# Performance work log

Hardware: AMD Instinct MI355X
Metric: run time of the kernel (lower is better)

## Reference

```python
import jax, jax.numpy as jnp
import numpy as np
from jax import lax

PS = 8  # patch size

def setup_inputs() -> dict:
    key = jax.random.key(0)
    ks = jax.random.split(key, 7)
    dim = 64
    B, H, W = 4, 256, 256
    x = jax.random.normal(ks[0], (B, dim, H, W), dtype=jnp.float32)
    # to_hidden: Conv2d(dim, 6*dim, k=1)
    w_hidden = jax.random.normal(ks[1], (6 * dim, dim, 1, 1), dtype=jnp.float32) * 0.05
    b_hidden = jax.random.normal(ks[2], (6 * dim,), dtype=jnp.float32) * 0.01
    # to_hidden_dw: depthwise Conv2d(6*dim, 6*dim, k=3, pad=1, groups=6*dim)
    w_dw = jax.random.normal(ks[3], (6 * dim, 1, 3, 3), dtype=jnp.float32) * 0.05
    b_dw = jax.random.normal(ks[4], (6 * dim,), dtype=jnp.float32) * 0.01
    # project_out: Conv2d(2*dim, dim, k=1)
    w_out = jax.random.normal(ks[5], (dim, 2 * dim, 1, 1), dtype=jnp.float32) * 0.05
    b_out = jax.random.normal(ks[6], (dim,), dtype=jnp.float32) * 0.01
    return {"x": x, "w_hidden": w_hidden, "b_hidden": b_hidden,
            "w_dw": w_dw, "b_dw": b_dw, "w_out": w_out, "b_out": b_out}

def _conv(x, w, groups=1, padding='VALID'):
    return lax.conv_general_dilated(
        x, w, window_strides=(1, 1), padding=padding,
        dimension_numbers=('NCHW', 'OIHW', 'NCHW'),
        feature_group_count=groups)

def reference(x, w_hidden, b_hidden, w_dw, b_dw, w_out, b_out):
    # 1x1 expansion to 6*dim channels
    hidden = _conv(x, w_hidden) + b_hidden[None, :, None, None]
    # 3x3 depthwise conv (groups == channels)
    dw = _conv(hidden, w_dw, groups=w_dw.shape[0], padding='SAME') + b_dw[None, :, None, None]
    q, k, v = jnp.split(dw, 3, axis=1)  # each (B, 2*dim, H, W)
    B, C, H, W = q.shape
    # raw reshape into (B,C,H/8,W/8,8,8) exactly as torch .reshape on contiguous NCHW
    q_patch = q.reshape(B, C, H // PS, W // PS, PS, PS)
    k_patch = k.reshape(B, C, H // PS, W // PS, PS, PS)
    q_fft = jnp.fft.rfft2(q_patch)
    k_fft = jnp.fft.rfft2(k_patch)
    out = jnp.fft.irfft2(q_fft * k_fft, s=(PS, PS))  # circular conv of q,k patches
    out = out.reshape(B, C, (H // PS) * PS, (W // PS) * PS)
    output = v * out
    output = _conv(output, w_out) + b_out[None, :, None, None]
    return output
```

## Files before the change

kernel.cpp:

```cpp
#include <hip/hip_runtime.h>

#define HW 65536
#define W_IMG 256
#define H_IMG 256
#define CIN 64
#define CHID 384
#define CQK 128

__global__ __launch_bounds__(256) void k1_expand(
    const float* __restrict__ x_base,
    const float* __restrict__ wh,
    const float* __restrict__ bh,
    float* __restrict__ hidden_base,
    size_t x_bstride, size_t hid_bstride)
{
    __shared__ float xs[32][256];
    const float* x = x_base + blockIdx.z * x_bstride;
    float* hidden  = hidden_base + blockIdx.z * hid_bstride;
    const int pxbase = blockIdx.x * 256;
    const int cobase = blockIdx.y * 64;
    const int tid  = threadIdx.x;
    const int lane = tid & 63;
    const int wq   = __builtin_amdgcn_readfirstlane(tid >> 6);
    const int px0  = lane * 4;
    const int cw   = cobase + wq * 16;

    float acc[16][4];
    #pragma unroll
    for (int i = 0; i < 16; ++i)
        #pragma unroll
        for (int j = 0; j < 4; ++j) acc[i][j] = 0.f;

    #pragma unroll
    for (int half = 0; half < 2; ++half) {
        const int cib = half * 32;
        if (half) __syncthreads();
        #pragma unroll
        for (int it = 0; it < 8; ++it) {
            int f4 = it * 256 + tid;
            int ci = f4 >> 6;
            int p4 = f4 & 63;
            *reinterpret_cast<float4*>(&xs[ci][p4 * 4]) =
                *reinterpret_cast<const float4*>(
                    &x[(size_t)(cib + ci) * HW + pxbase + p4 * 4]);
        }
        __syncthreads();

        for (int ci4 = 0; ci4 < 32; ci4 += 4) {
            float4 xv[4];
            #pragma unroll
            for (int u = 0; u < 4; ++u)
                xv[u] = *reinterpret_cast<const float4*>(&xs[ci4 + u][px0]);
            #pragma unroll
            for (int g = 0; g < 4; ++g) {
                #pragma unroll
                for (int i = 0; i < 4; ++i) {
                    float4 wv = *reinterpret_cast<const float4*>(
                        &wh[(size_t)(cw + g * 4 + i) * CIN + cib + ci4]);
                    float wu[4] = {wv.x, wv.y, wv.z, wv.w};
                    #pragma unroll
                    for (int u = 0; u < 4; ++u) {
                        acc[g * 4 + i][0] += wu[u] * xv[u].x;
                        acc[g * 4 + i][1] += wu[u] * xv[u].y;
                        acc[g * 4 + i][2] += wu[u] * xv[u].z;
                        acc[g * 4 + i][3] += wu[u] * xv[u].w;
                    }
                }
            }
        }
    }

    #pragma unroll
    for (int i = 0; i < 16; ++i) {
        int co = cw + i;
        float b = bh[co];
        float4 o;
        o.x = acc[i][0] + b; o.y = acc[i][1] + b;
        o.z = acc[i][2] + b; o.w = acc[i][3] + b;
        *reinterpret_cast<float4*>(&hidden[(size_t)co * HW + pxbase + px0]) = o;
    }
}

__global__ __launch_bounds__(256) void k2_fused(
    const float* __restrict__ hidden_base,
    const float* __restrict__ wdw,
    const float* __restrict__ bdw,
    float* __restrict__ vout_base,
    size_t hid_bstride, size_t vout_bstride)
{
    __shared__ float stg[2][10][260];
    __shared__ float qk[2][8][4][68];

    const float* hidden = hidden_base + blockIdx.z * hid_bstride;
    float* vout         = vout_base + blockIdx.z * vout_bstride;

    const int c  = blockIdx.y;
    const int r0 = blockIdx.x * 8;
    const int tid = threadIdx.x;

    #pragma unroll
    for (int it = 0; it < 5; ++it) {
        int f4  = it * 256 + tid;
        int ch  = f4 / 640;
        int rem = f4 - ch * 640;
        int lr  = rem >> 6;
        int p4  = rem & 63;
        int gr  = r0 - 1 + lr;
        float4 v = make_float4(0.f, 0.f, 0.f, 0.f);
        if ((unsigned)gr < H_IMG)
            v = *reinterpret_cast<const float4*>(
                &hidden[(size_t)(c + ch * CQK) * HW + (size_t)gr * W_IMG + p4 * 4]);
        *reinterpret_cast<float4*>(&stg[ch][lr][p4 * 4]) = v;
    }
    __syncthreads();

    const int w = tid;
    const int segw = w >> 6;
    const int tw   = w & 63;
    #pragma unroll
    for (int ch = 0; ch < 2; ++ch) {
        const float* wv = wdw + (c + ch * CQK) * 9;
        const float bias = bdw[c + ch * CQK];
        const float w0 = wv[0], w1 = wv[1], w2 = wv[2];
        const float w3 = wv[3], w4 = wv[4], w5 = wv[5];
        const float w6 = wv[6], w7 = wv[7], w8 = wv[8];
        const float* S = &stg[ch][0][0];

        float am, a0, ap, bm, b0, bp;
        a0 = S[w];
        am = (w > 0)   ? S[w - 1] : 0.f;
        ap = (w < 255) ? S[w + 1] : 0.f;
        b0 = S[260 + w];
        bm = (w > 0)   ? S[260 + w - 1] : 0.f;
        bp = (w < 255) ? S[260 + w + 1] : 0.f;

        #pragma unroll
        for (int r = 0; r < 8; ++r) {
            const float* Sr = S + (r + 2) * 260;
            float c0 = Sr[w];
            float cm = (w > 0)   ? Sr[w - 1] : 0.f;
            float cp = (w < 255) ? Sr[w + 1] : 0.f;
            float a = bias + am * w0 + a0 * w1 + ap * w2
                           + bm * w3 + b0 * w4 + bp * w5
                           + cm * w6 + c0 * w7 + cp * w8;
            qk[ch][r][segw][tw] = a;
            am = bm; a0 = b0; ap = bp;
            bm = cm; b0 = c0; bp = cp;
        }
    }
    __syncthreads();

    const int row = tid >> 5;
    const int seg = (tid >> 3) & 3;
    const int i   = tid & 7;
    const int gr  = r0 + row;
    const int wp0 = seg * 64 + i * 8;

    const float* hbv = hidden + (size_t)(c + 2 * CQK) * HW;
    float4 hv[3][2];
    float  hm[3], hp[3];
    #pragma unroll
    for (int ky = 0; ky < 3; ++ky) {
        int grr = gr + ky - 1;
        hv[ky][0] = make_float4(0.f, 0.f, 0.f, 0.f);
        hv[ky][1] = make_float4(0.f, 0.f, 0.f, 0.f);
        hm[ky] = 0.f; hp[ky] = 0.f;
        if ((unsigned)grr < H_IMG) {
            const float* rb = hbv + (size_t)grr * W_IMG;
            hv[ky][0] = *reinterpret_cast<const float4*>(&rb[wp0]);
            hv[ky][1] = *reinterpret_cast<const float4*>(&rb[wp0 + 4]);
            hm[ky] = (wp0 > 0)   ? rb[wp0 - 1] : 0.f;
            hp[ky] = (wp0 < 248) ? rb[wp0 + 8] : 0.f;
        }
    }

    const float* qb = &qk[0][row][seg][0];
    const float* kb = &qk[1][row][seg][0];

    float acc[8];
    #pragma unroll
    for (int j = 0; j < 8; ++j) acc[j] = 0.f;

    #pragma unroll
    for (int s = 0; s < 8; ++s) {
        int qr = (i - s) & 7;
        float4 ka = *reinterpret_cast<const float4*>(&kb[s * 8]);
        float4 kc = *reinterpret_cast<const float4*>(&kb[s * 8 + 4]);
        float4 qa = *reinterpret_cast<const float4*>(&qb[qr * 8]);
        float4 qc = *reinterpret_cast<const float4*>(&qb[qr * 8 + 4]);
        float kr[8] = {ka.x, ka.y, ka.z, ka.w, kc.x, kc.y, kc.z, kc.w};
        float qv[8] = {qa.x, qa.y, qa.z, qa.w, qc.x, qc.y, qc.z, qc.w};
        #pragma unroll
        for (int t = 0; t < 8; ++t)
            #pragma unroll
            for (int j = 0; j < 8; ++j)
                acc[j] += kr[t] * qv[(j - t) & 7];
    }

    const float* wvv = wdw + (c + 2 * CQK) * 9;
    const float vbias = bdw[c + 2 * CQK];
    float vc[8];
    #pragma unroll
    for (int j = 0; j < 8; ++j) vc[j] = vbias;
    #pragma unroll
    for (int ky = 0; ky < 3; ++ky) {
        float kw0 = wvv[ky * 3], kw1 = wvv[ky * 3 + 1], kw2 = wvv[ky * 3 + 2];
        float h[10];
        h[0] = hm[ky];
        h[1] = hv[ky][0].x; h[2] = hv[ky][0].y; h[3] = hv[ky][0].z; h[4] = hv[ky][0].w;
        h[5] = hv[ky][1].x; h[6] = hv[ky][1].y; h[7] = hv[ky][1].z; h[8] = hv[ky][1].w;
        h[9] = hp[ky];
        #pragma unroll
        for (int j = 0; j < 8; ++j)
            vc[j] += h[j] * kw0 + h[j + 1] * kw1 + h[j + 2] * kw2;
    }

    float* dst = &vout[(size_t)c * HW + (size_t)gr * W_IMG + wp0];
    float4 o0, o1;
    o0.x = acc[0] * vc[0]; o0.y = acc[1] * vc[1];
    o0.z = acc[2] * vc[2]; o0.w = acc[3] * vc[3];
    o1.x = acc[4] * vc[4]; o1.y = acc[5] * vc[5];
    o1.z = acc[6] * vc[6]; o1.w = acc[7] * vc[7];
    *reinterpret_cast<float4*>(dst)     = o0;
    *reinterpret_cast<float4*>(dst + 4) = o1;
}

__global__ __launch_bounds__(256) void k3_project(
    const float* __restrict__ vout_base,
    const float* __restrict__ wo,
    const float* __restrict__ bo,
    float* __restrict__ out_base,
    size_t vout_bstride, size_t out_bstride)
{
    __shared__ float vsh[CQK][64];
    const float* vout = vout_base + blockIdx.z * vout_bstride;
    float* out        = out_base + blockIdx.z * out_bstride;
    const int pxbase = blockIdx.x * 64;
    const int tid  = threadIdx.x;
    const int lane = tid & 63;
    const int wq   = __builtin_amdgcn_readfirstlane(tid >> 6);
    const int cw   = wq * 16;

    #pragma unroll
    for (int it = 0; it < 8; ++it) {
        int f4 = it * 256 + tid;
        int cc = f4 >> 4;
        int p4 = f4 & 15;
        *reinterpret_cast<float4*>(&vsh[cc][p4 * 4]) =
            *reinterpret_cast<const float4*>(&vout[(size_t)cc * HW + pxbase + p4 * 4]);
    }
    __syncthreads();

    float acc[16];
    #pragma unroll
    for (int i = 0; i < 16; ++i) acc[i] = 0.f;

    for (int cc4 = 0; cc4 < CQK; cc4 += 4) {
        float xv[4];
        #pragma unroll
        for (int u = 0; u < 4; ++u)
            xv[u] = vsh[cc4 + u][lane];
        #pragma unroll
        for (int g = 0; g < 4; ++g) {
            #pragma unroll
            for (int i = 0; i < 4; ++i) {
                float4 wv = *reinterpret_cast<const float4*>(
                    &wo[(size_t)(cw + g * 4 + i) * CQK + cc4]);
                acc[g * 4 + i] += wv.x * xv[0] + wv.y * xv[1]
                                + wv.z * xv[2] + wv.w * xv[3];
            }
        }
    }

    #pragma unroll
    for (int i = 0; i < 16; ++i) {
        int co = cw + i;
        out[(size_t)co * HW + pxbase + lane] = acc[i] + bo[co];
    }
}

extern "C" void kernel_launch(void* const* d_in, const int* in_sizes, int n_in,
                              void* d_out, int out_size, void* d_ws, size_t ws_size,
                              hipStream_t stream) {
    const float* x   = (const float*)d_in[0];
    const float* wh  = (const float*)d_in[1];
    const float* bh  = (const float*)d_in[2];
    const float* wdw = (const float*)d_in[3];
    const float* bdw = (const float*)d_in[4];
    const float* wo  = (const float*)d_in[5];
    const float* bo  = (const float*)d_in[6];
    float* out = (float*)d_out;

    const size_t n_hid  = (size_t)CHID * HW;
    const size_t n_vout = (size_t)CQK * HW;
    const size_t n_x    = (size_t)CIN * HW;

    if (ws_size >= 4 * (n_hid + n_vout) * sizeof(float)) {
        float* hidden = (float*)d_ws;
        float* vout   = hidden + 4 * n_hid;
        k1_expand <<<dim3(HW / 256, CHID / 64, 4), 256, 0, stream>>>(
            x, wh, bh, hidden, n_x, n_hid);
        k2_fused  <<<dim3(H_IMG / 8, CQK, 4),      256, 0, stream>>>(
            hidden, wdw, bdw, vout, n_hid, n_vout);
        k3_project<<<dim3(HW / 64, 1, 4),          256, 0, stream>>>(
            vout, wo, bo, out, n_vout, n_x);
    } else {
        float* hidden = (float*)d_ws;
        float* vout   = hidden + n_hid;
        for (int b = 0; b < 4; ++b) {
            const float* xb = x + (size_t)b * n_x;
            float* ob       = out + (size_t)b * n_x;
            k1_expand <<<dim3(HW / 256, CHID / 64, 1), 256, 0, stream>>>(
                xb, wh, bh, hidden, 0, 0);
            k2_fused  <<<dim3(H_IMG / 8, CQK, 1),      256, 0, stream>>>(
                hidden, wdw, bdw, vout, 0, 0);
            k3_project<<<dim3(HW / 64, 1, 1),          256, 0, stream>>>(
                vout, wo, bo, ob, 0, 0);
        }
    }
}
```

Measured before the change: 464.2 us.

## Drop LDS staging in 1x1 convs and read inputs directly from global

Both pointwise conv kernels (expand and project) stop staging input tiles in shared memory with barriers. Each thread now loads its float4 pixel columns straight from global memory inside the channel loop. The project kernel is also reworked so each thread computes 4 pixels × 16 output channels, with 256 pixels per block and a quarter as many blocks, plus float4 stores. This removes LDS traffic and synchronization, relying on L1/L2 caching for the reuse across the four waves that share pixels. The trade-off is more global load instructions and higher register pressure.

```diff
diff --git a/kernel.cpp b/kernel.cpp
--- a/kernel.cpp
+++ b/kernel.cpp
@@ -14,7 +14,6 @@
     float* __restrict__ hidden_base,
     size_t x_bstride, size_t hid_bstride)
 {
-    __shared__ float xs[32][256];
     const float* x = x_base + blockIdx.z * x_bstride;
     float* hidden  = hidden_base + blockIdx.z * hid_bstride;
     const int pxbase = blockIdx.x * 256;
@@ -22,7 +21,7 @@
     const int tid  = threadIdx.x;
     const int lane = tid & 63;
     const int wq   = __builtin_amdgcn_readfirstlane(tid >> 6);
-    const int px0  = lane * 4;
+    const int px   = pxbase + lane * 4;
     const int cw   = cobase + wq * 16;
 
     float acc[16][4];
@@ -31,41 +30,23 @@
         #pragma unroll
         for (int j = 0; j < 4; ++j) acc[i][j] = 0.f;
 
-    #pragma unroll
-    for (int half = 0; half < 2; ++half) {
-        const int cib = half * 32;
-        if (half) __syncthreads();
-        #pragma unroll
-        for (int it = 0; it < 8; ++it) {
-            int f4 = it * 256 + tid;
-            int ci = f4 >> 6;
-            int p4 = f4 & 63;
-            *reinterpret_cast<float4*>(&xs[ci][p4 * 4]) =
-                *reinterpret_cast<const float4*>(
-                    &x[(size_t)(cib + ci) * HW + pxbase + p4 * 4]);
-        }
-        __syncthreads();
-
-        for (int ci4 = 0; ci4 < 32; ci4 += 4) {
-            float4 xv[4];
+    #pragma unroll 2
+    for (int ci4 = 0; ci4 < CIN; ci4 += 4) {
+        float4 xv[4];
+        #pragma unroll
+        for (int u = 0; u < 4; ++u)
+            xv[u] = *reinterpret_cast<const float4*>(&x[(size_t)(ci4 + u) * HW + px]);
+        #pragma unroll
+        for (int i = 0; i < 16; ++i) {
+            float4 wv = *reinterpret_cast<const float4*>(
+                &wh[(size_t)(cw + i) * CIN + ci4]);
+            float wu[4] = {wv.x, wv.y, wv.z, wv.w};
             #pragma unroll
-            for (int u = 0; u < 4; ++u)
-                xv[u] = *reinterpret_cast<const float4*>(&xs[ci4 + u][px0]);
-            #pragma unroll
-            for (int g = 0; g < 4; ++g) {
-                #pragma unroll
-                for (int i = 0; i < 4; ++i) {
-                    float4 wv = *reinterpret_cast<const float4*>(
-                        &wh[(size_t)(cw + g * 4 + i) * CIN + cib + ci4]);
-                    float wu[4] = {wv.x, wv.y, wv.z, wv.w};
-                    #pragma unroll
-                    for (int u = 0; u < 4; ++u) {
-                        acc[g * 4 + i][0] += wu[u] * xv[u].x;
-                        acc[g * 4 + i][1] += wu[u] * xv[u].y;
-                        acc[g * 4 + i][2] += wu[u] * xv[u].z;
-                        acc[g * 4 + i][3] += wu[u] * xv[u].w;
-                    }
-                }
+            for (int u = 0; u < 4; ++u) {
+                acc[i][0] += wu[u] * xv[u].x;
+                acc[i][1] += wu[u] * xv[u].y;
+                acc[i][2] += wu[u] * xv[u].z;
+                acc[i][3] += wu[u] * xv[u].w;
             }
         }
     }
@@ -77,7 +58,7 @@
         float4 o;
         o.x = acc[i][0] + b; o.y = acc[i][1] + b;
         o.z = acc[i][2] + b; o.w = acc[i][3] + b;
-        *reinterpret_cast<float4*>(&hidden[(size_t)co * HW + pxbase + px0]) = o;
+        *reinterpret_cast<float4*>(&hidden[(size_t)co * HW + px]) = o;
     }
 }
 
@@ -232,42 +213,38 @@
     float* __restrict__ out_base,
     size_t vout_bstride, size_t out_bstride)
 {
-    __shared__ float vsh[CQK][64];
     const float* vout = vout_base + blockIdx.z * vout_bstride;
     float* out        = out_base + blockIdx.z * out_bstride;
-    const int pxbase = blockIdx.x * 64;
+    const int pxbase = blockIdx.x * 256;
     const int tid  = threadIdx.x;
     const int lane = tid & 63;
     const int wq   = __builtin_amdgcn_readfirstlane(tid >> 6);
+    const int px   = pxbase + lane * 4;
     const int cw   = wq * 16;
 
-    #pragma unroll
-    for (int it = 0; it < 8; ++it) {
-        int f4 = it * 256 + tid;
-        int cc = f4 >> 4;
-        int p4 = f4 & 15;
-        *reinterpret_cast<float4*>(&vsh[cc][p4 * 4]) =
-            *reinterpret_cast<const float4*>(&vout[(size_t)cc * HW + pxbase + p4 * 4]);
-    }
-    __syncthreads();
-
-    float acc[16];
-    #pragma unroll
-    for (int i = 0; i < 16; ++i) acc[i] = 0.f;
-
+    float acc[16][4];
+    #pragma unroll
+    for (int i = 0; i < 16; ++i)
+        #pragma unroll
+        for (int j = 0; j < 4; ++j) acc[i][j] = 0.f;
+
+    #pragma unroll 2
     for (int cc4 = 0; cc4 < CQK; cc4 += 4) {
-        float xv[4];
+        float4 xv[4];
         #pragma unroll
         for (int u = 0; u < 4; ++u)
-            xv[u] = vsh[cc4 + u][lane];
-        #pragma unroll
-        for (int g = 0; g < 4; ++g) {
+            xv[u] = *reinterpret_cast<const float4*>(&vout[(size_t)(cc4 + u) * HW + px]);
+        #pragma unroll
+        for (int i = 0; i < 16; ++i) {
+            float4 wv = *reinterpret_cast<const float4*>(
+                &wo[(size_t)(cw + i) * CQK + cc4]);
+            float wu[4] = {wv.x, wv.y, wv.z, wv.w};
             #pragma unroll
-            for (int i = 0; i < 4; ++i) {
-                float4 wv = *reinterpret_cast<const float4*>(
-                    &wo[(size_t)(cw + g * 4 + i) * CQK + cc4]);
-                acc[g * 4 + i] += wv.x * xv[0] + wv.y * xv[1]
-                                + wv.z * xv[2] + wv.w * xv[3];
+            for (int u = 0; u < 4; ++u) {
+                acc[i][0] += wu[u] * xv[u].x;
+                acc[i][1] += wu[u] * xv[u].y;
+                acc[i][2] += wu[u] * xv[u].z;
+                acc[i][3] += wu[u] * xv[u].w;
             }
         }
     }
@@ -275,7 +252,11 @@
     #pragma unroll
     for (int i = 0; i < 16; ++i) {
         int co = cw + i;
-        out[(size_t)co * HW + pxbase + lane] = acc[i] + bo[co];
+        float b = bo[co];
+        float4 o;
+        o.x = acc[i][0] + b; o.y = acc[i][1] + b;
+        o.z = acc[i][2] + b; o.w = acc[i][3] + b;
+        *reinterpret_cast<float4*>(&out[(size_t)co * HW + px]) = o;
     }
 }
 
@@ -302,7 +283,7 @@
             x, wh, bh, hidden, n_x, n_hid);
         k2_fused  <<<dim3(H_IMG / 8, CQK, 4),      256, 0, stream>>>(
             hidden, wdw, bdw, vout, n_hid, n_vout);
-        k3_project<<<dim3(HW / 64, 1, 4),          256, 0, stream>>>(
+        k3_project<<<dim3(HW / 256, 1, 4),         256, 0, stream>>>(
             vout, wo, bo, out, n_vout, n_x);
     } else {
         float* hidden = (float*)d_ws;
@@ -314,7 +295,7 @@
                 xb, wh, bh, hidden, 0, 0);
             k2_fused  <<<dim3(H_IMG / 8, CQK, 1),      256, 0, stream>>>(
                 hidden, wdw, bdw, vout, 0, 0);
-            k3_project<<<dim3(HW / 64, 1, 1),          256, 0, stream>>>(
+            k3_project<<<dim3(HW / 256, 1, 1),         256, 0, stream>>>(
                 vout, wo, bo, ob, 0, 0);
         }
     }
```

Measured after the change: 420.1 us. -9.5%, faster.
